# Optimization experiments

Measured on AMD Instinct MI355X. Metric: run time of the kernel, lower is better.

Reference implementation:

```python
import jax, jax.numpy as jnp
import numpy as np

GAMMA = 0.8
LOSS_WEIGHT = 1.0


def charbonnier(x, alpha=0.25, eps=1e-9):
    return jnp.power(x * x + eps * eps, alpha)


def grid_sample_zeros(img, xp, yp):
    # img [C,H,W]; xp,yp [H,W] absolute pixel coords. Bilinear, zeros padding,
    # matching F.grid_sample(..., align_corners=True) after coord unnormalization.
    H, W = img.shape[1], img.shape[2]
    x0 = jnp.floor(xp); y0 = jnp.floor(yp)
    x1 = x0 + 1.0;      y1 = y0 + 1.0
    wx1 = xp - x0; wx0 = 1.0 - wx1
    wy1 = yp - y0; wy0 = 1.0 - wy1

    def tap(xi, yi, w):
        valid = (xi >= 0) & (xi <= W - 1) & (yi >= 0) & (yi <= H - 1)
        xc = jnp.clip(xi, 0, W - 1).astype(jnp.int32)
        yc = jnp.clip(yi, 0, H - 1).astype(jnp.int32)
        return img[:, yc, xc] * (w * valid)[None]  # [C,H,W]

    return tap(x0, y0, wx0 * wy0) + tap(x1, y0, wx1 * wy0) + \
           tap(x0, y1, wx0 * wy1) + tap(x1, y1, wx1 * wy1)


def stn_warp(flow, frm):
    # flow [B,2,H,W], frm [B,3,H,W] (same resolution -> interpolate is identity)
    B, _, H, W = flow.shape
    xx = jnp.arange(W, dtype=flow.dtype)[None, :]
    yy = jnp.arange(H, dtype=flow.dtype)[:, None]
    gx = (flow[:, 0] + xx) * (2.0 / W) - 1.0   # normalized grid, as in _stn
    gy = (flow[:, 1] + yy) * (2.0 / H) - 1.0
    xp = (gx + 1.0) * 0.5 * (W - 1)            # align_corners=True unnormalize
    yp = (gy + 1.0) * 0.5 * (H - 1)
    return jax.vmap(grid_sample_zeros)(frm, xp, yp)


def smoothness_loss(flow):
    B = flow.shape[0]
    v = jnp.pad(flow[:, :, 1:, :], ((0, 0), (0, 0), (0, 1), (0, 0)))
    h = jnp.pad(flow[:, :, :, 1:], ((0, 0), (0, 0), (0, 0), (0, 1)))
    s = charbonnier(flow - v) + charbonnier(flow - h)
    return jnp.sum(jnp.sum(s, axis=1) / 2.0) / B


def photometric_loss(warped, frm0):
    p = jnp.sum(charbonnier(warped - frm0), axis=1) / 3.0
    return jnp.sum(p) / frm0.shape[0]


def keypoint_gt_flow(kps, B, H, W):
    # Vectorized version of the per-keypoint python scatter loop.
    kps0 = kps[:, 0]  # [B,J,2] (x,y)
    kps1 = kps[:, 1]
    disps = kps1 - kps0
    valid = ((kps0[..., 0] >= 0) & (kps0[..., 1] >= 0) &
             (kps1[..., 0] >= 0) & (kps1[..., 1] >= 0) &
             (kps0[..., 0] < W) & (kps0[..., 1] < H) &
             (kps1[..., 0] < W) & (kps1[..., 1] < H))
    # invalid keypoints are routed to the padding row/col (H, W) and sliced off
    xi = jnp.where(valid, jnp.floor(kps0[..., 0]), W).astype(jnp.int32)
    yi = jnp.where(valid, jnp.floor(kps0[..., 1]), H).astype(jnp.int32)
    b = jnp.broadcast_to(jnp.arange(B)[:, None], xi.shape)
    gt = jnp.zeros((B, H + 1, W + 1, 2), kps.dtype).at[b, yi, xi].set(disps)
    return jnp.transpose(gt[:, :H, :W, :], (0, 3, 1, 2))  # [B,2,H,W]


def reference(pred_flows, kps, frm0, frm1):
    N, B, _, H, W = pred_flows.shape
    weights = [GAMMA ** (N - i - 1) for i in range(N)]

    # ---- supervised keypoint-flow EPE ----
    gt_flow = keypoint_gt_flow(kps, B, H, W)
    mask = (jnp.sqrt(jnp.sum(gt_flow ** 2, axis=1)) > 0).astype(pred_flows.dtype)
    denom = jnp.maximum(jnp.sum(mask), 1.0)
    sup = 0.0
    for i in range(N):
        epe = jnp.sqrt(jnp.sum((pred_flows[i] - gt_flow) ** 2, axis=1))  # [B,H,W]
        sup = sup + weights[i] * jnp.sum(epe * mask) / denom
    sup = sup * LOSS_WEIGHT

    # ---- unsupervised photometric + smoothness ----
    unsup = 0.0
    for i in range(N):
        warped = stn_warp(pred_flows[i], frm1)
        unsup = unsup + weights[i] * photometric_loss(warped, frm0)
        unsup = unsup + weights[i] * smoothness_loss(pred_flows[i])

    return sup + unsup


def setup_inputs() -> dict:
    key = jax.random.key(0)
    k1, k2, k3, k4 = jax.random.split(key, 4)
    N, B, H, W, J = 5, 16, 384, 384, 17
    pred_flows = jax.random.normal(k1, (N, B, 2, H, W), jnp.float32) * 2.0
    # keypoints in pixel coords, with a few slightly out-of-range (negative / >= W,H)
    kps = (jax.random.uniform(k2, (B, 2, J, 2), jnp.float32)
           * jnp.array([W * 1.05, H * 1.05], jnp.float32) - 8.0)
    frm0 = jax.random.uniform(k3, (B, 3, H, W), jnp.float32)
    frm1 = jax.random.uniform(k4, (B, 3, H, W), jnp.float32)
    return {"pred_flows": pred_flows, "kps": kps, "frm0": frm0, "frm1": frm1}
```

## Files before the change

kernel.cpp:

```cpp
#include <hip/hip_runtime.h>

#define NF 5
#define NB 16
#define NH 384
#define NW 384
#define NJ 17
#define HW (NH * NW)
#define PW (NW + 3)
#define PH (NH + 3)
#define PHW (PH * PW)
#define NPIX (NB * HW)
#define PACK_TOTAL (NB * PHW)
#define NTHREADS4 (NF * NB * NH * (NW / 4))
#define UNSUP4_BLOCKS (NTHREADS4 / 256)
#define UNSUP1_BLOCKS ((NF * NB * HW) / 256)

__device__ __forceinline__ float charb(float x) {
    return __builtin_amdgcn_sqrtf(__builtin_amdgcn_sqrtf(fmaf(x, x, 1e-18f)));
}
__device__ __forceinline__ unsigned int packrgb(float r, float g, float b) {
    unsigned int er = (unsigned int)fmaf(r, 2047.f, 0.5f);
    unsigned int eg = (unsigned int)fmaf(g, 2047.f, 0.5f);
    unsigned int eb = (unsigned int)fmaf(b, 1023.f, 0.5f);
    return er | (eg << 11) | (eb << 22);
}
__device__ __forceinline__ float upk_r(unsigned int u) {
    return (float)(u & 2047u) * (1.f / 2047.f);
}
__device__ __forceinline__ float upk_g(unsigned int u) {
    return (float)((u >> 11) & 2047u) * (1.f / 2047.f);
}
__device__ __forceinline__ float upk_b(unsigned int u) {
    return (float)(u >> 22) * (1.f / 1023.f);
}


__global__ __launch_bounds__(256)
void repack_kp_kernel(const float* __restrict__ frm1, const float* __restrict__ frm0,
                      const float* __restrict__ kps, const float* __restrict__ pf,
                      float* __restrict__ ws, unsigned int* __restrict__ packed1,
                      unsigned int* __restrict__ packed0, int do_pack) {
    int g = blockIdx.x * 256 + threadIdx.x;
    if (do_pack) {
        if (g < PACK_TOTAL) {
            int b = g / PHW;
            int r = g - b * PHW;
            int py = r / PW;
            int px = r - py * PW;
            int x = px - 1, y = py - 1;
            unsigned int v = 0u;
            if (x >= 0 && x < NW && y >= 0 && y < NH) {
                const float* s = frm1 + (size_t)b * 3 * HW + y * NW + x;
                v = packrgb(s[0], s[HW], s[2 * HW]);
            }
            packed1[g] = v;
        }
        if (g < NPIX) {
            int b = g / HW;
            int o = g - b * HW;
            const float* s = frm0 + (size_t)b * 3 * HW + o;
            packed0[g] = packrgb(s[0], s[HW], s[2 * HW]);
        }
    }
    if (blockIdx.x == 0) {
        int t = threadIdx.x;
        __shared__ int cnt;
        __shared__ int ebase[NB * NJ];
        __shared__ float edx[NB * NJ], edy[NB * NJ];
        if (t == 0) cnt = 0;
        __syncthreads();
        for (int q = t; q < NB * NJ; q += 256) {
            int b = q / NJ, j = q - b * NJ;
            const float* k0 = kps + ((b * 2 + 0) * NJ + j) * 2;
            const float* k1 = kps + ((b * 2 + 1) * NJ + j) * 2;
            float x0 = k0[0], y0 = k0[1], x1 = k1[0], y1 = k1[1];
            bool valid = x0 >= 0.f && y0 >= 0.f && x1 >= 0.f && y1 >= 0.f &&
                         x0 < (float)NW && y0 < (float)NH &&
                         x1 < (float)NW && y1 < (float)NH;
            float dx = x1 - x0, dy = y1 - y0;
            if (valid && (dx != 0.f || dy != 0.f)) {
                int s = atomicAdd(&cnt, 1);
                ebase[s] = (b * 2) * HW + (int)floorf(y0) * NW + (int)floorf(x0);
                edx[s] = dx; edy[s] = dy;
            }
        }
        __syncthreads();
        int n = cnt;
        float local = 0.f;
        for (int q = t; q < n * NF; q += 256) {
            int e = q / NF, i = q - e * NF;
            float wt = (i == 0) ? 0.4096f : (i == 1) ? 0.512f :
                       (i == 2) ? 0.64f  : (i == 3) ? 0.8f   : 1.0f;
            int off = ebase[e] + i * (NB * 2 * HW);
            float ex = pf[off] - edx[e];
            float ey = pf[off + HW] - edy[e];
            local += wt * sqrtf(fmaf(ex, ex, ey * ey));
        }
        for (int o = 32; o > 0; o >>= 1) local += __shfl_down(local, o, 64);
        __shared__ float ssum[4];
        int lane = t & 63, wid = t >> 6;
        if (lane == 0) ssum[wid] = local;
        __syncthreads();
        if (t == 0) {
            ws[0] = ssum[0] + ssum[1] + ssum[2] + ssum[3];
            ws[1] = (float)n;
        }
    }
}

__global__ __launch_bounds__(256, 6)
void unsup4_kernel(const float* __restrict__ pf, const unsigned int* __restrict__ packed1,
                   const unsigned int* __restrict__ packed0, float* __restrict__ partials) {
    const int idx = blockIdx.x * 256 + threadIdx.x;
    const int w4 = idx % (NW / 4);
    int q = idx / (NW / 4);
    const int i = q % NF;
    q = q / NF;
    const int b = q & (NB - 1);
    const int h = q >> 4;
    const int w0 = w4 * 4;
    const int off = h * NW + w0;
    const float SC = (float)(NW - 1) / (float)NW;

    const uint4 f0 = *reinterpret_cast<const uint4*>(packed0 + (size_t)b * HW + off);

    const float* fb = pf + (size_t)((i * NB + b) * 2) * HW + off;
    const float4 fx4 = *(const float4*)fb;
    const float4 fy4 = *(const float4*)(fb + HW);
    float4 dnx4 = make_float4(0.f, 0.f, 0.f, 0.f);
    float4 dny4 = make_float4(0.f, 0.f, 0.f, 0.f);
    if (h < NH - 1) {
        dnx4 = *(const float4*)(fb + NW);
        dny4 = *(const float4*)(fb + NW + HW);
    }
    float rtx = 0.f, rty = 0.f;
    if (w0 + 4 < NW) { rtx = fb[4]; rty = fb[HW + 4]; }

    const float fxa[4] = {fx4.x, fx4.y, fx4.z, fx4.w};
    const float fya[4] = {fy4.x, fy4.y, fy4.z, fy4.w};

    const unsigned int* pk = packed1 + (size_t)b * PHW;
    int pbase[4];
    float wx1a[4], wy1a[4];
#pragma unroll
    for (int k = 0; k < 4; ++k) {
        float xp = (fxa[k] + (float)(w0 + k)) * SC;
        float yp = (fya[k] + (float)h) * SC;
        xp = fminf(fmaxf(xp, -1.0f), 384.0f);
        yp = fminf(fmaxf(yp, -1.0f), 384.0f);
        float x0f = floorf(xp), y0f = floorf(yp);
        wx1a[k] = xp - x0f;
        wy1a[k] = yp - y0f;
        pbase[k] = ((int)y0f + 1) * PW + ((int)x0f + 1);
    }
    unsigned int t00[4], t10[4], t01[4], t11[4];
#pragma unroll
    for (int k = 0; k < 4; ++k) {
        t00[k] = pk[pbase[k]];
        t10[k] = pk[pbase[k] + 1];
        t01[k] = pk[pbase[k] + PW];
        t11[k] = pk[pbase[k] + PW + 1];
    }

    const float rxa[4] = {fx4.y, fx4.z, fx4.w, rtx};
    const float rya[4] = {fy4.y, fy4.z, fy4.w, rty};
    const float dnxa[4] = {dnx4.x, dnx4.y, dnx4.z, dnx4.w};
    const float dnya[4] = {dny4.x, dny4.y, dny4.z, dny4.w};
    float smooth = 0.f;
#pragma unroll
    for (int k = 0; k < 4; ++k) {
        smooth += charb(fxa[k] - dnxa[k]) + charb(fya[k] - dnya[k]) +
                  charb(fxa[k] - rxa[k]) + charb(fya[k] - rya[k]);
    }

    const unsigned int f0a[4] = {f0.x, f0.y, f0.z, f0.w};
    float phot = 0.f;
#pragma unroll
    for (int k = 0; k < 4; ++k) {
        float wx1 = wx1a[k], wx0 = 1.f - wx1;
        float wy1 = wy1a[k], wy0 = 1.f - wy1;
        float w00 = wx0 * wy0, w10 = wx1 * wy0, w01 = wx0 * wy1, w11 = wx1 * wy1;
        float s0 = w00 * upk_r(t00[k]) + w10 * upk_r(t10[k]) +
                   w01 * upk_r(t01[k]) + w11 * upk_r(t11[k]);
        float s1 = w00 * upk_g(t00[k]) + w10 * upk_g(t10[k]) +
                   w01 * upk_g(t01[k]) + w11 * upk_g(t11[k]);
        float s2 = w00 * upk_b(t00[k]) + w10 * upk_b(t10[k]) +
                   w01 * upk_b(t01[k]) + w11 * upk_b(t11[k]);
        phot += charb(s0 - upk_r(f0a[k])) + charb(s1 - upk_g(f0a[k])) +
                charb(s2 - upk_b(f0a[k]));
    }

    float wt = (i == 0) ? 0.4096f : (i == 1) ? 0.512f :
               (i == 2) ? 0.64f  : (i == 3) ? 0.8f   : 1.0f;
    float local = wt * fmaf(phot, (1.f / 3.f), smooth * 0.5f);

    for (int o = 32; o > 0; o >>= 1) local += __shfl_down(local, o, 64);
    __shared__ float ssum[4];
    int lane = threadIdx.x & 63, wid = threadIdx.x >> 6;
    if (lane == 0) ssum[wid] = local;
    __syncthreads();
    if (threadIdx.x == 0) {
        partials[blockIdx.x] = ssum[0] + ssum[1] + ssum[2] + ssum[3];
    }
}

__global__ __launch_bounds__(256, 8)
void unsup1_kernel(const float* __restrict__ pf, const float* __restrict__ frm0,
                   const float* __restrict__ frm1, float* __restrict__ partials) {
    const int idx = blockIdx.x * 256 + threadIdx.x;
    const int w = idx % NW;
    int q = idx / NW;
    const int i = q % NF;
    q = q / NF;
    const int b = q & (NB - 1);
    const int h = q >> 4;
    const int off = h * NW + w;
    const float SC = (float)(NW - 1) / (float)NW;
    const float* f0b = frm0 + b * 3 * HW + off;
    const float c0 = f0b[0], c1 = f0b[HW], c2 = f0b[2 * HW];
    const float* fb = pf + (size_t)((i * NB + b) * 2) * HW + off;
    const float fx = fb[0], fy = fb[HW];
    float dnx = 0.f, dny = 0.f, rtx = 0.f, rty = 0.f;
    if (h < NH - 1) { dnx = fb[NW]; dny = fb[NW + HW]; }
    if (w < NW - 1) { rtx = fb[1];  rty = fb[HW + 1]; }
    float smooth = charb(fx - dnx) + charb(fy - dny) + charb(fx - rtx) + charb(fy - rty);
    float xp = (fx + (float)w) * SC, yp = (fy + (float)h) * SC;
    float x0f = floorf(xp), y0f = floorf(yp);
    float wx1 = xp - x0f, wx0 = 1.f - wx1, wy1 = yp - y0f, wy0 = 1.f - wy1;
    bool vx0 = (x0f >= 0.f) && (x0f <= (float)(NW - 1));
    bool vx1 = (x0f >= -1.f) && (x0f <= (float)(NW - 2));
    bool vy0 = (y0f >= 0.f) && (y0f <= (float)(NH - 1));
    bool vy1 = (y0f >= -1.f) && (y0f <= (float)(NH - 2));
    float m00 = (vx0 && vy0) ? wx0 * wy0 : 0.f;
    float m10 = (vx1 && vy0) ? wx1 * wy0 : 0.f;
    float m01 = (vx0 && vy1) ? wx0 * wy1 : 0.f;
    float m11 = (vx1 && vy1) ? wx1 * wy1 : 0.f;
    int x0i = min(max((int)x0f, 0), NW - 1);
    int y0i = min(max((int)y0f, 0), NH - 1);
    int x1i = min(x0i + 1, NW - 1);
    int y1i = min(y0i + 1, NH - 1);
    const float* img = frm1 + b * 3 * HW;
    int i00 = y0i * NW + x0i, i10 = y0i * NW + x1i;
    int i01 = y1i * NW + x0i, i11 = y1i * NW + x1i;
    float s0 = m00 * img[i00] + m10 * img[i10] + m01 * img[i01] + m11 * img[i11];
    float s1 = m00 * img[HW + i00] + m10 * img[HW + i10] + m01 * img[HW + i01] + m11 * img[HW + i11];
    float s2 = m00 * img[2 * HW + i00] + m10 * img[2 * HW + i10] + m01 * img[2 * HW + i01] + m11 * img[2 * HW + i11];
    float phot = charb(s0 - c0) + charb(s1 - c1) + charb(s2 - c2);
    float wt = (i == 0) ? 0.4096f : (i == 1) ? 0.512f :
               (i == 2) ? 0.64f  : (i == 3) ? 0.8f   : 1.0f;
    float local = wt * fmaf(phot, (1.f / 3.f), smooth * 0.5f);
    for (int o = 32; o > 0; o >>= 1) local += __shfl_down(local, o, 64);
    __shared__ float ssum[4];
    int lane = threadIdx.x & 63, wid = threadIdx.x >> 6;
    if (lane == 0) ssum[wid] = local;
    __syncthreads();
    if (threadIdx.x == 0) partials[blockIdx.x] = ssum[0] + ssum[1] + ssum[2] + ssum[3];
}

__global__ __launch_bounds__(1024)
void final_kernel(const float* __restrict__ ws, const float* __restrict__ partials,
                  float* __restrict__ out, int nparts) {
    float local = 0.f;
    for (int q = threadIdx.x; q < nparts; q += 1024) local += partials[q];
    for (int o = 32; o > 0; o >>= 1) local += __shfl_down(local, o, 64);
    __shared__ float ssum[16];
    int lane = threadIdx.x & 63, wid = threadIdx.x >> 6;
    if (lane == 0) ssum[wid] = local;
    __syncthreads();
    if (threadIdx.x == 0) {
        float uns = 0.f;
        #pragma unroll
        for (int k = 0; k < 16; ++k) uns += ssum[k];
        float denom = fmaxf(ws[1], 1.f);
        out[0] = uns * (1.f / (float)NB) + ws[0] / denom;
    }
}

extern "C" void kernel_launch(void* const* d_in, const int* in_sizes, int n_in,
                              void* d_out, int out_size, void* d_ws, size_t ws_size,
                              hipStream_t stream) {
    const float* pf   = (const float*)d_in[0];
    const float* kps  = (const float*)d_in[1];
    const float* frm0 = (const float*)d_in[2];
    const float* frm1 = (const float*)d_in[3];
    float* out = (float*)d_out;
    float* ws  = (float*)d_ws;

    char* base = (char*)d_ws;
    unsigned int* packed1 = (unsigned int*)(base + 64);
    unsigned int* packed0 = (unsigned int*)(base + 64 + (size_t)PACK_TOTAL * 4);
    float* partials4 = (float*)(base + 64 + (size_t)PACK_TOTAL * 4 + (size_t)NPIX * 4);

    const size_t need = 64 + (size_t)PACK_TOTAL * 4 + (size_t)NPIX * 4 +
                        (size_t)UNSUP4_BLOCKS * 4;
    if (ws_size >= need) {
        repack_kp_kernel<<<(PACK_TOTAL + 255) / 256, 256, 0, stream>>>(
            frm1, frm0, kps, pf, ws, packed1, packed0, 1);
        unsup4_kernel<<<UNSUP4_BLOCKS, 256, 0, stream>>>(pf, packed1, packed0, partials4);
        final_kernel<<<1, 1024, 0, stream>>>(ws, partials4, out, UNSUP4_BLOCKS);
    } else {
        float* partials1 = ws + 16;
        repack_kp_kernel<<<1, 256, 0, stream>>>(frm1, frm0, kps, pf, ws,
                                                packed1, packed0, 0);
        unsup1_kernel<<<UNSUP1_BLOCKS, 256, 0, stream>>>(pf, frm0, frm1, partials1);
        final_kernel<<<1, 1024, 0, stream>>>(ws, partials1, out, UNSUP1_BLOCKS);
    }
}
```

Before: 225.7 us.

## Stage a packed frame row window in shared memory for warp gathers

The unsupervised kernel is restructured so that each block handles one (batch, row) pair across all five flow levels. It first loads a 12-row window of the packed frm1 image into LDS, then serves the bilinear taps from that window and falls back to global memory when the flow lands outside it. Because the five flow levels share one staged window, gather traffic to global memory and L2 should drop. In exchange every block pays a load and a barrier before it starts, 32 of its 512 threads sit idle, and large flows still take the divergent global path.

New measurement: 232.7 us. +3.1%, slower.

```diff
diff --git a/kernel.cpp b/kernel.cpp
--- a/kernel.cpp
+++ b/kernel.cpp
@@ -11,8 +11,9 @@
 #define PHW (PH * PW)
 #define NPIX (NB * HW)
 #define PACK_TOTAL (NB * PHW)
-#define NTHREADS4 (NF * NB * NH * (NW / 4))
-#define UNSUP4_BLOCKS (NTHREADS4 / 256)
+#define WROWS 12
+#define WSIZE (WROWS * PW)
+#define SBLOCKS (NB * NH)
 #define UNSUP1_BLOCKS ((NF * NB * HW) / 256)
 
 __device__ __forceinline__ float charb(float x) {
@@ -108,99 +109,107 @@
     }
 }
 
-__global__ __launch_bounds__(256, 6)
-void unsup4_kernel(const float* __restrict__ pf, const unsigned int* __restrict__ packed1,
-                   const unsigned int* __restrict__ packed0, float* __restrict__ partials) {
-    const int idx = blockIdx.x * 256 + threadIdx.x;
-    const int w4 = idx % (NW / 4);
-    int q = idx / (NW / 4);
-    const int i = q % NF;
-    q = q / NF;
-    const int b = q & (NB - 1);
-    const int h = q >> 4;
-    const int w0 = w4 * 4;
-    const int off = h * NW + w0;
-    const float SC = (float)(NW - 1) / (float)NW;
-
-    const uint4 f0 = *reinterpret_cast<const uint4*>(packed0 + (size_t)b * HW + off);
-
-    const float* fb = pf + (size_t)((i * NB + b) * 2) * HW + off;
-    const float4 fx4 = *(const float4*)fb;
-    const float4 fy4 = *(const float4*)(fb + HW);
-    float4 dnx4 = make_float4(0.f, 0.f, 0.f, 0.f);
-    float4 dny4 = make_float4(0.f, 0.f, 0.f, 0.f);
-    if (h < NH - 1) {
-        dnx4 = *(const float4*)(fb + NW);
-        dny4 = *(const float4*)(fb + NW + HW);
-    }
-    float rtx = 0.f, rty = 0.f;
-    if (w0 + 4 < NW) { rtx = fb[4]; rty = fb[HW + 4]; }
-
-    const float fxa[4] = {fx4.x, fx4.y, fx4.z, fx4.w};
-    const float fya[4] = {fy4.x, fy4.y, fy4.z, fy4.w};
+__global__ __launch_bounds__(512, 8)
+void unsup_stage_kernel(const float* __restrict__ pf,
+                        const unsigned int* __restrict__ packed1,
+                        const unsigned int* __restrict__ packed0,
+                        float* __restrict__ partials) {
+    __shared__ unsigned int win[WSIZE];
+    const int t = threadIdx.x;
+    const int blk = blockIdx.x;
+    const int h = blk % NH;
+    const int b = blk / NH;
+    const int lo = min(max(h - 5, 0), PH - WROWS);
 
     const unsigned int* pk = packed1 + (size_t)b * PHW;
-    int pbase[4];
-    float wx1a[4], wy1a[4];
+    for (int s = t; s < WSIZE; s += 512) win[s] = pk[lo * PW + s];
+    __syncthreads();
+
+    float local = 0.f;
+    if (t < 480) {
+        const int w4 = t % 96;
+        const int i = t / 96;
+        const int w0 = w4 * 4;
+        const int off = h * NW + w0;
+        const float SC = (float)(NW - 1) / (float)NW;
+
+        const uint4 f0 = *reinterpret_cast<const uint4*>(packed0 + (size_t)b * HW + off);
+
+        const float* fb = pf + (size_t)((i * NB + b) * 2) * HW + off;
+        const float4 fx4 = *(const float4*)fb;
+        const float4 fy4 = *(const float4*)(fb + HW);
+        float4 dnx4 = make_float4(0.f, 0.f, 0.f, 0.f);
+        float4 dny4 = make_float4(0.f, 0.f, 0.f, 0.f);
+        if (h < NH - 1) {
+            dnx4 = *(const float4*)(fb + NW);
+            dny4 = *(const float4*)(fb + NW + HW);
+        }
+        float rtx = 0.f, rty = 0.f;
+        if (w0 + 4 < NW) { rtx = fb[4]; rty = fb[HW + 4]; }
+
+        const float fxa[4] = {fx4.x, fx4.y, fx4.z, fx4.w};
+        const float fya[4] = {fy4.x, fy4.y, fy4.z, fy4.w};
+        const float rxa[4] = {fx4.y, fx4.z, fx4.w, rtx};
+        const float rya[4] = {fy4.y, fy4.z, fy4.w, rty};
+        const float dnxa[4] = {dnx4.x, dnx4.y, dnx4.z, dnx4.w};
+        const float dnya[4] = {dny4.x, dny4.y, dny4.z, dny4.w};
+        const unsigned int f0a[4] = {f0.x, f0.y, f0.z, f0.w};
+
+        float smooth = 0.f, phot = 0.f;
 #pragma unroll
-    for (int k = 0; k < 4; ++k) {
-        float xp = (fxa[k] + (float)(w0 + k)) * SC;
-        float yp = (fya[k] + (float)h) * SC;
-        xp = fminf(fmaxf(xp, -1.0f), 384.0f);
-        yp = fminf(fmaxf(yp, -1.0f), 384.0f);
-        float x0f = floorf(xp), y0f = floorf(yp);
-        wx1a[k] = xp - x0f;
-        wy1a[k] = yp - y0f;
-        pbase[k] = ((int)y0f + 1) * PW + ((int)x0f + 1);
-    }
-    unsigned int t00[4], t10[4], t01[4], t11[4];
-#pragma unroll
-    for (int k = 0; k < 4; ++k) {
-        t00[k] = pk[pbase[k]];
-        t10[k] = pk[pbase[k] + 1];
-        t01[k] = pk[pbase[k] + PW];
-        t11[k] = pk[pbase[k] + PW + 1];
-    }
-
-    const float rxa[4] = {fx4.y, fx4.z, fx4.w, rtx};
-    const float rya[4] = {fy4.y, fy4.z, fy4.w, rty};
-    const float dnxa[4] = {dnx4.x, dnx4.y, dnx4.z, dnx4.w};
-    const float dnya[4] = {dny4.x, dny4.y, dny4.z, dny4.w};
-    float smooth = 0.f;
-#pragma unroll
-    for (int k = 0; k < 4; ++k) {
-        smooth += charb(fxa[k] - dnxa[k]) + charb(fya[k] - dnya[k]) +
-                  charb(fxa[k] - rxa[k]) + charb(fya[k] - rya[k]);
-    }
-
-    const unsigned int f0a[4] = {f0.x, f0.y, f0.z, f0.w};
-    float phot = 0.f;
-#pragma unroll
-    for (int k = 0; k < 4; ++k) {
-        float wx1 = wx1a[k], wx0 = 1.f - wx1;
-        float wy1 = wy1a[k], wy0 = 1.f - wy1;
-        float w00 = wx0 * wy0, w10 = wx1 * wy0, w01 = wx0 * wy1, w11 = wx1 * wy1;
-        float s0 = w00 * upk_r(t00[k]) + w10 * upk_r(t10[k]) +
-                   w01 * upk_r(t01[k]) + w11 * upk_r(t11[k]);
-        float s1 = w00 * upk_g(t00[k]) + w10 * upk_g(t10[k]) +
-                   w01 * upk_g(t01[k]) + w11 * upk_g(t11[k]);
-        float s2 = w00 * upk_b(t00[k]) + w10 * upk_b(t10[k]) +
-                   w01 * upk_b(t01[k]) + w11 * upk_b(t11[k]);
-        phot += charb(s0 - upk_r(f0a[k])) + charb(s1 - upk_g(f0a[k])) +
-                charb(s2 - upk_b(f0a[k]));
-    }
-
-    float wt = (i == 0) ? 0.4096f : (i == 1) ? 0.512f :
-               (i == 2) ? 0.64f  : (i == 3) ? 0.8f   : 1.0f;
-    float local = wt * fmaf(phot, (1.f / 3.f), smooth * 0.5f);
+        for (int k = 0; k < 4; ++k) {
+            smooth += charb(fxa[k] - dnxa[k]) + charb(fya[k] - dnya[k]) +
+                      charb(fxa[k] - rxa[k]) + charb(fya[k] - rya[k]);
+
+            float xp = (fxa[k] + (float)(w0 + k)) * SC;
+            float yp = (fya[k] + (float)h) * SC;
+            xp = fminf(fmaxf(xp, -1.0f), 384.0f);
+            yp = fminf(fmaxf(yp, -1.0f), 384.0f);
+            float x0f = floorf(xp), y0f = floorf(yp);
+            float wx1 = xp - x0f, wx0 = 1.f - wx1;
+            float wy1 = yp - y0f, wy0 = 1.f - wy1;
+            int px0 = (int)x0f + 1;
+            int py0 = (int)y0f + 1;
+            int wr = py0 - lo;
+            unsigned int t00, t10, t01, t11;
+            if ((unsigned)wr <= (unsigned)(WROWS - 2)) {
+                int l = wr * PW + px0;
+                t00 = win[l];
+                t10 = win[l + 1];
+                t01 = win[l + PW];
+                t11 = win[l + PW + 1];
+            } else {
+                int g = py0 * PW + px0;
+                t00 = pk[g];
+                t10 = pk[g + 1];
+                t01 = pk[g + PW];
+                t11 = pk[g + PW + 1];
+            }
+            float w00 = wx0 * wy0, w10 = wx1 * wy0, w01 = wx0 * wy1, w11 = wx1 * wy1;
+            float s0 = w00 * upk_r(t00) + w10 * upk_r(t10) +
+                       w01 * upk_r(t01) + w11 * upk_r(t11);
+            float s1 = w00 * upk_g(t00) + w10 * upk_g(t10) +
+                       w01 * upk_g(t01) + w11 * upk_g(t11);
+            float s2 = w00 * upk_b(t00) + w10 * upk_b(t10) +
+                       w01 * upk_b(t01) + w11 * upk_b(t11);
+            phot += charb(s0 - upk_r(f0a[k])) + charb(s1 - upk_g(f0a[k])) +
+                    charb(s2 - upk_b(f0a[k]));
+        }
+        float wt = (i == 0) ? 0.4096f : (i == 1) ? 0.512f :
+                   (i == 2) ? 0.64f  : (i == 3) ? 0.8f   : 1.0f;
+        local = wt * fmaf(phot, (1.f / 3.f), smooth * 0.5f);
+    }
 
     for (int o = 32; o > 0; o >>= 1) local += __shfl_down(local, o, 64);
-    __shared__ float ssum[4];
-    int lane = threadIdx.x & 63, wid = threadIdx.x >> 6;
+    __shared__ float ssum[8];
+    int lane = t & 63, wid = t >> 6;
     if (lane == 0) ssum[wid] = local;
     __syncthreads();
-    if (threadIdx.x == 0) {
-        partials[blockIdx.x] = ssum[0] + ssum[1] + ssum[2] + ssum[3];
+    if (t == 0) {
+        float s = 0.f;
+        #pragma unroll
+        for (int k = 0; k < 8; ++k) s += ssum[k];
+        partials[blockIdx.x] = s;
     }
 }
 
@@ -289,15 +298,15 @@
     char* base = (char*)d_ws;
     unsigned int* packed1 = (unsigned int*)(base + 64);
     unsigned int* packed0 = (unsigned int*)(base + 64 + (size_t)PACK_TOTAL * 4);
-    float* partials4 = (float*)(base + 64 + (size_t)PACK_TOTAL * 4 + (size_t)NPIX * 4);
+    float* partialsS = (float*)(base + 64 + (size_t)PACK_TOTAL * 4 + (size_t)NPIX * 4);
 
     const size_t need = 64 + (size_t)PACK_TOTAL * 4 + (size_t)NPIX * 4 +
-                        (size_t)UNSUP4_BLOCKS * 4;
+                        (size_t)SBLOCKS * 4;
     if (ws_size >= need) {
         repack_kp_kernel<<<(PACK_TOTAL + 255) / 256, 256, 0, stream>>>(
             frm1, frm0, kps, pf, ws, packed1, packed0, 1);
-        unsup4_kernel<<<UNSUP4_BLOCKS, 256, 0, stream>>>(pf, packed1, packed0, partials4);
-        final_kernel<<<1, 1024, 0, stream>>>(ws, partials4, out, UNSUP4_BLOCKS);
+        unsup_stage_kernel<<<SBLOCKS, 512, 0, stream>>>(pf, packed1, packed0, partialsS);
+        final_kernel<<<1, 1024, 0, stream>>>(ws, partialsS, out, SBLOCKS);
     } else {
         float* partials1 = ws + 16;
         repack_kp_kernel<<<1, 256, 0, stream>>>(frm1, frm0, kps, pf, ws,
```
